# Kernel tuning notes

Hardware: AMD Instinct MI355X
Metric: run time of the kernel (lower is better)

Reference implementation:

```python
import jax, jax.numpy as jnp
import numpy as np

CHANNELS = 1024
N_HEADS = 16
N_EMBD = 512
H_DIM = CHANNELS // N_HEADS


def setup_inputs() -> dict:
    key = jax.random.key(0)
    ks = jax.random.split(key, 10)
    b, hw = 16, 4096
    s = 0.02
    return {
        "x": jax.random.normal(ks[0], (b, hw, CHANNELS), dtype=jnp.float32),
        "p": jax.random.normal(ks[1], (b, 77, N_EMBD), dtype=jnp.float32),
        "Wq": jax.random.normal(ks[2], (CHANNELS, CHANNELS), dtype=jnp.float32) * s,
        "bq": jnp.zeros((CHANNELS,), dtype=jnp.float32),
        "Wk": jax.random.normal(ks[3], (N_EMBD, CHANNELS), dtype=jnp.float32) * s,
        "bk": jnp.zeros((CHANNELS,), dtype=jnp.float32),
        "Wv": jax.random.normal(ks[4], (N_EMBD, CHANNELS), dtype=jnp.float32) * s,
        "bv": jnp.zeros((CHANNELS,), dtype=jnp.float32),
        "Ww": jax.random.normal(ks[5], (CHANNELS, CHANNELS), dtype=jnp.float32) * s,
        "bw": jnp.zeros((CHANNELS,), dtype=jnp.float32),
    }


def reference(x, p, Wq, bq, Wk, bk, Wv, bv, Ww, bw):
    b, hw, c = x.shape
    # Linear projections (torch Linear: y = x @ W^T + b; here weights stored as (in, out))
    q = x @ Wq + bq                      # (b, hw, c)
    k = p @ Wk + bk                      # (b, 77, c)
    v = p @ Wv + bv                      # (b, 77, c)
    q = q.reshape(b, hw, N_HEADS, H_DIM)
    k = k.reshape(b, 77, N_HEADS, H_DIM)
    v = v.reshape(b, 77, N_HEADS, H_DIM)
    scale = 1.0 / jnp.sqrt(jnp.asarray(H_DIM, dtype=x.dtype))
    # scores: (b, heads, hw, 77)
    scores = jnp.einsum("bqhd,bkhd->bhqk", q, k) * scale
    attn = jax.nn.softmax(scores, axis=-1)
    out = jnp.einsum("bhqk,bkhd->bqhd", attn, v).reshape(b, hw, c)
    return out @ Ww + bw
```

## Files before the change

kernel.cpp:

```cpp
#include <hip/hip_runtime.h>
#include <cstdint>
#include <type_traits>

typedef uint16_t u16;
typedef uint32_t u32;
typedef __attribute__((ext_vector_type(4))) float f32x4;
typedef __attribute__((ext_vector_type(8))) __bf16 vbf8;
typedef __attribute__((ext_vector_type(8))) short vs8;

template <typename T, typename = void>
struct CanMfma : std::false_type {};
template <typename T>
struct CanMfma<T, std::void_t<decltype(__builtin_amdgcn_mfma_f32_16x16x32_bf16(
    std::declval<T>(), std::declval<T>(), std::declval<f32x4>(), 0, 0, 0))>>
    : std::true_type {};
typedef std::conditional_t<CanMfma<vbf8>::value, vbf8, vs8> frag_t;

__device__ __forceinline__ f32x4 mfma_bf16(frag_t a, frag_t b, f32x4 c) {
  return __builtin_amdgcn_mfma_f32_16x16x32_bf16(a, b, c, 0, 0, 0);
}

__device__ __forceinline__ u16 f2bf(float f) {
  u32 u = __builtin_bit_cast(u32, f);
  u32 r = (u + 0x7FFFu + ((u >> 16) & 1u)) >> 16;
  return (u16)r;
}

__device__ __forceinline__ void gload_lds16(const void* g, void* l) {
  __builtin_amdgcn_global_load_lds(
      (const __attribute__((address_space(1))) void*)g,
      (__attribute__((address_space(3))) void*)l, 16, 0, 0);
}

__global__ __launch_bounds__(256) void cast_f32_bf16(
    const float* __restrict__ in, u16* __restrict__ out, int n8) {
  int i = blockIdx.x * 256 + threadIdx.x;
  const int stride = gridDim.x * 256;
  for (; i < n8; i += stride) {
    const float4 a  = ((const float4*)in)[(size_t)i * 2];
    const float4 b2 = ((const float4*)in)[(size_t)i * 2 + 1];
    uint4 o;
    o.x = (u32)f2bf(a.x)  | ((u32)f2bf(a.y)  << 16);
    o.y = (u32)f2bf(a.z)  | ((u32)f2bf(a.w)  << 16);
    o.z = (u32)f2bf(b2.x) | ((u32)f2bf(b2.y) << 16);
    o.w = (u32)f2bf(b2.z) | ((u32)f2bf(b2.w) << 16);
    ((uint4*)out)[(size_t)i] = o;
  }
}

__global__ __launch_bounds__(256) void transpose_cast(
    const float* __restrict__ in, u16* __restrict__ out, int K, int N) {
  __shared__ float tile[32][33];
  const int k0 = blockIdx.x * 32, n0 = blockIdx.y * 32;
  const int tr = threadIdx.x >> 5, tc = threadIdx.x & 31;
#pragma unroll
  for (int i = 0; i < 4; ++i)
    tile[tr + i * 8][tc] = in[(size_t)(k0 + tr + i * 8) * N + (n0 + tc)];
  __syncthreads();
#pragma unroll
  for (int i = 0; i < 4; ++i)
    out[(size_t)(n0 + tr + i * 8) * K + (k0 + tc)] = f2bf(tile[tc][tr + i * 8]);
}

template <bool OUT_BF16>
__global__ __launch_bounds__(256) void gemm_bt(
    const u16* __restrict__ A, const u16* __restrict__ Bt,
    const float* __restrict__ bias, void* __restrict__ Cout,
    int M, int N, int K, int Mtiles, int Ntiles) {
  __shared__ char Al[2][128 * 32 * 2];
  __shared__ char Bl[2][128 * 32 * 2];

  const int nwg = Mtiles * Ntiles;
  int bid = (int)blockIdx.x;
  bid = (bid & 7) * (nwg >> 3) + (bid >> 3);
  const int mt = bid / Ntiles, nt = bid % Ntiles;
  const int m0 = mt * 128, n0 = nt * 128;

  const int tid = (int)threadIdx.x;
  const int lane = tid & 63;
  const int wv = tid >> 6;
  const int wm = wv & 1, wn = wv >> 1;
  const int lr = lane & 15, lg = lane >> 4;
  const int rsub = lane >> 2;
  const int slot = lane & 3;
  const int rb0 = n0 + rsub;

  auto stage = [&](int buf, int t) {
    const int k0 = t << 5;
#pragma unroll
    for (int c = 0; c < 2; ++c) {
      const int ci = c * 4 + wv;
      int rra = m0 + ci * 16 + rsub;
      if (rra >= M) rra = M - 1;
      gload_lds16(A + (size_t)rra * K + k0 + slot * 8, Al[buf] + ci * 1024);
      const int rrb = rb0 + ci * 16;
      gload_lds16(Bt + (size_t)rrb * K + k0 + slot * 8, Bl[buf] + ci * 1024);
    }
  };

  f32x4 zero4 = {0.f, 0.f, 0.f, 0.f};
  f32x4 acc[4][4];
#pragma unroll
  for (int i = 0; i < 4; ++i)
#pragma unroll
    for (int j = 0; j < 4; ++j) acc[i][j] = zero4;

  const int nk = K >> 5;
  int cur = 0;
  stage(0, 0);
  __syncthreads();

  for (int t = 0; t < nk; ++t) {
    if (t + 1 < nk) stage(cur ^ 1, t + 1);
    frag_t af[4], bf[4];
#pragma unroll
    for (int i = 0; i < 4; ++i) {
      af[i] = *(const frag_t*)(Al[cur] + (wm * 64 + i * 16 + lr) * 64 + lg * 16);
      bf[i] = *(const frag_t*)(Bl[cur] + (wn * 64 + i * 16 + lr) * 64 + lg * 16);
    }
#pragma unroll
    for (int i = 0; i < 4; ++i)
#pragma unroll
      for (int j = 0; j < 4; ++j)
        acc[i][j] = mfma_bf16(af[i], bf[j], acc[i][j]);
    __syncthreads();
    cur ^= 1;
  }

#pragma unroll
  for (int j = 0; j < 4; ++j) {
    const int col = n0 + wn * 64 + j * 16 + lr;
    const float bv = bias[col];
#pragma unroll
    for (int i = 0; i < 4; ++i) {
      const int rbase = m0 + wm * 64 + i * 16 + lg * 4;
#pragma unroll
      for (int r = 0; r < 4; ++r) {
        const int row = rbase + r;
        const float val = acc[i][j][r] + bv;
        if constexpr (OUT_BF16) {
          u32 me = f2bf(val);
          u32 other = __shfl_xor(me, 1);
          if ((lane & 1) == 0 && row < M) {
            *(u32*)((u16*)Cout + (size_t)row * N + col) = me | (other << 16);
          }
        } else {
          if (row < M) ((float*)Cout)[(size_t)row * N + col] = val;
        }
      }
    }
  }
}

template <bool OUT_BF16>
__global__ __launch_bounds__(512) void gemm256(
    const u16* __restrict__ A, const u16* __restrict__ Bt,
    const float* __restrict__ bias, void* __restrict__ Cout,
    int M, int N, int K) {
  __shared__ u16 Al[2][256 * 64];
  __shared__ u16 Bl[2][256 * 64];

  const int Ntiles = N >> 8;
  const int nwg = (M >> 8) * Ntiles;
  int bid = (int)blockIdx.x;
  bid = (bid & 7) * (nwg >> 3) + (bid >> 3);
  const int mt = bid / Ntiles, ntl = bid % Ntiles;
  const int m0 = mt << 8, n0 = ntl << 8;

  const int tid = (int)threadIdx.x;
  const int lane = tid & 63;
  const int wid = tid >> 6;
  const int wm = wid >> 2, wn = wid & 3;
  const int lr = lane & 15, lg = lane >> 4;
  const int lrx = lr & 7;

  const int chunk = wid * 2;
  const int srow = lane >> 3;
  const int sslot = (lane & 7) ^ srow;
  const u16* Abase = A + (size_t)(m0 + chunk * 8 + srow) * K + sslot * 8;
  const u16* Bbase = Bt + (size_t)(n0 + chunk * 8 + srow) * K + sslot * 8;
  const int ldsChunkByte = (chunk * 8) * 128;

  auto stA = [&](u16* dst, int h, int t) {
    const u16* g = Abase + (size_t)(h << 7) * K + (t << 6);
    char* l = (char*)dst + (h << 14) + ldsChunkByte;
    gload_lds16(g, l);
    gload_lds16(g + ((size_t)K << 3), l + 1024);
  };
  auto stB = [&](u16* dst, int h, int t) {
    const u16* g = Bbase + (size_t)(h << 7) * K + (t << 6);
    char* l = (char*)dst + (h << 14) + ldsChunkByte;
    gload_lds16(g, l);
    gload_lds16(g + ((size_t)K << 3), l + 1024);
  };

  auto ldsF = [&](const u16* base, int row, int ks) -> frag_t {
    return *(const frag_t*)(base + (size_t)row * 64 + ((((ks) << 2) + lg) ^ lrx) * 8);
  };

  f32x4 zero4 = {0.f, 0.f, 0.f, 0.f};
  f32x4 acc[8][4];
#pragma unroll
  for (int i = 0; i < 8; ++i)
#pragma unroll
    for (int j = 0; j < 4; ++j) acc[i][j] = zero4;

  const int nt = K >> 6;
  const int ar0 = wm * 128 + lr;
  const int br0 = wn * 64 + lr;

  stB(&Bl[0][0], 0, 0); stB(&Bl[0][0], 1, 0);
  stA(&Al[0][0], 0, 0); stA(&Al[0][0], 1, 0);
  stB(&Bl[1][0], 0, 1); stB(&Bl[1][0], 1, 1);
  stA(&Al[1][0], 0, 1); stA(&Al[1][0], 1, 1);
  asm volatile("s_waitcnt vmcnt(8)" ::: "memory");
  __builtin_amdgcn_s_barrier();

  for (int t = 0; t < nt; ++t) {
    const int cur = t & 1;
    const u16* al = &Al[cur][0];
    const u16* bl = &Bl[cur][0];
    if (t >= 1 && t + 1 < nt) {
      u16* alN = &Al[cur ^ 1][0];
      u16* blN = &Bl[cur ^ 1][0];
      stB(blN, 0, t + 1); stB(blN, 1, t + 1);
      stA(alN, 0, t + 1); stA(alN, 1, t + 1);
    }
#pragma unroll
    for (int ks = 0; ks < 2; ++ks) {
      frag_t a[8], b[4];
#pragma unroll
      for (int i = 0; i < 8; ++i) a[i] = ldsF(al, ar0 + i * 16, ks);
#pragma unroll
      for (int j = 0; j < 4; ++j) b[j] = ldsF(bl, br0 + j * 16, ks);
#pragma unroll
      for (int i = 0; i < 8; ++i)
#pragma unroll
        for (int j = 0; j < 4; ++j)
          acc[i][j] = mfma_bf16(a[i], b[j], acc[i][j]);
    }
    if (t + 1 < nt) {
      asm volatile("s_waitcnt vmcnt(0)" ::: "memory");
      __builtin_amdgcn_s_barrier();
    }
  }

  float bvv[4];
#pragma unroll
  for (int bj = 0; bj < 4; ++bj) bvv[bj] = bias[n0 + wn * 64 + bj * 16 + lr];
#pragma unroll
  for (int ai = 0; ai < 8; ++ai) {
    const int rbase = m0 + wm * 128 + ai * 16 + lg * 4;
#pragma unroll
    for (int rr = 0; rr < 4; ++rr) {
      const int row = rbase + rr;
#pragma unroll
      for (int bj = 0; bj < 4; ++bj) {
        const int cb = n0 + wn * 64 + bj * 16;
        const float val = acc[ai][bj][rr] + bvv[bj];
        if constexpr (OUT_BF16) {
          u32 me = f2bf(val);
          u32 d0 = me | (__shfl_xor(me, 1) << 16);
          u32 d1 = __shfl_xor(d0, 2);
          if ((lane & 3) == 0) {
            uint2 o; o.x = d0; o.y = d1;
            *(uint2*)((u16*)Cout + (size_t)row * N + cb + (lr & 12)) = o;
          }
        } else {
          float v0 = val;
          float v1 = __shfl_xor(v0, 1);
          float v2 = __shfl_xor(v0, 2);
          float v3 = __shfl_xor(v1, 2);
          if ((lane & 3) == 0) {
            float4 o; o.x = v0; o.y = v1; o.z = v2; o.w = v3;
            *(float4*)((float*)Cout + (size_t)row * N + cb + (lr & 12)) = o;
          }
        }
      }
    }
  }
}

__global__ __launch_bounds__(256) void attn_kernel(
    const u16* __restrict__ Q, const u16* __restrict__ K,
    const u16* __restrict__ V, u16* __restrict__ O) {
  __shared__ u16 Kl[96][72];
  __shared__ u16 Vt[64][104];

  const int bid = blockIdx.x;
  const int qt = bid & 63;
  const int h = (bid >> 6) & 15;
  const int b = bid >> 10;
  const int tid = threadIdx.x;

#pragma unroll
  for (int it = 0; it < 3; ++it) {
    const int idx = tid + it * 256;
    const int key = idx >> 3, s = idx & 7;
    uint4 val{0u, 0u, 0u, 0u};
    if (key < 77)
      val = *(const uint4*)(K + ((size_t)(b * 77 + key)) * 1024 + h * 64 + s * 8);
    *(uint4*)(&Kl[key][s * 8]) = val;
  }
#pragma unroll
  for (int it = 0; it < 3; ++it) {
    const int idx = tid + it * 256;
    if (idx < 616) {
      const int key = idx >> 3, s = idx & 7;
      const uint4 v4 =
          *(const uint4*)(V + ((size_t)(b * 77 + key)) * 1024 + h * 64 + s * 8);
      const u16* e = (const u16*)&v4;
#pragma unroll
      for (int j = 0; j < 8; ++j) Vt[s * 8 + j][key] = e[j];
    }
  }
#pragma unroll
  for (int it = 0; it < 5; ++it) {
    const int idx = tid + it * 256;
    if (idx < 1216) {
      const int d = idx / 19, kk = 77 + idx % 19;
      Vt[d][kk] = 0;
    }
  }
  __syncthreads();

  const int lane = tid & 63;
  const int wv = tid >> 6;
  const int lr = lane & 15;
  const int lg = lane >> 4;

  const size_t qrow = (size_t)(b * 4096 + qt * 64 + wv * 16 + lr) * 1024 + h * 64;
  frag_t qf[2];
#pragma unroll
  for (int ks = 0; ks < 2; ++ks)
    qf[ks] = *(const frag_t*)(Q + qrow + ks * 32 + lg * 8);

  f32x4 zero4 = {0.f, 0.f, 0.f, 0.f};
  f32x4 sa[5] = {zero4, zero4, zero4, zero4, zero4};
#pragma unroll
  for (int ks = 0; ks < 2; ++ks) {
#pragma unroll
    for (int kt = 0; kt < 5; ++kt) {
      frag_t kf = *(const frag_t*)(&Kl[kt * 16 + lr][ks * 32 + lg * 8]);
      sa[kt] = mfma_bf16(kf, qf[ks], sa[kt]);
    }
  }

  float p[5][4];
  float mx = -3.0e38f;
#pragma unroll
  for (int kt = 0; kt < 5; ++kt)
#pragma unroll
    for (int r = 0; r < 4; ++r) {
      const int key = kt * 16 + lg * 4 + r;
      float s = sa[kt][r] * 0.125f;
      if (key >= 77) s = -3.0e38f;
      p[kt][r] = s;
      mx = fmaxf(mx, s);
    }
  mx = fmaxf(mx, __shfl_xor(mx, 16));
  mx = fmaxf(mx, __shfl_xor(mx, 32));
  float sum = 0.f;
#pragma unroll
  for (int kt = 0; kt < 5; ++kt)
#pragma unroll
    for (int r = 0; r < 4; ++r) {
      const float e = __expf(p[kt][r] - mx);
      p[kt][r] = e;
      sum += e;
    }
  sum += __shfl_xor(sum, 16);
  sum += __shfl_xor(sum, 32);
  const float rden = 1.0f / sum;
#pragma unroll
  for (int kt = 0; kt < 5; ++kt)
#pragma unroll
    for (int r = 0; r < 4; ++r) p[kt][r] *= rden;

  union FP { frag_t v; u16 e[8]; };
  frag_t pa[3];
#pragma unroll
  for (int kb = 0; kb < 3; ++kb) {
    FP f;
#pragma unroll
    for (int j = 0; j < 8; ++j) {
      const int kt = 2 * kb + (j >> 2);
      f.e[j] = (kt < 5) ? f2bf(p[kt][j & 3]) : (u16)0;
    }
    pa[kb] = f.v;
  }

  f32x4 oa[4] = {zero4, zero4, zero4, zero4};
#pragma unroll
  for (int nt = 0; nt < 4; ++nt) {
    const int d = nt * 16 + lr;
#pragma unroll
    for (int kb = 0; kb < 3; ++kb) {
      const int key0 = kb * 32 + lg * 4;
      FP vb;
      *(uint2*)(&vb.e[0]) = *(const uint2*)(&Vt[d][key0]);
      *(uint2*)(&vb.e[4]) = *(const uint2*)(&Vt[d][key0 + 16]);
      oa[nt] = mfma_bf16(pa[kb], vb.v, oa[nt]);
    }
  }

#pragma unroll
  for (int nt = 0; nt < 4; ++nt)
#pragma unroll
    for (int r = 0; r < 4; ++r) {
      const int qr = wv * 16 + lg * 4 + r;
      u32 me = f2bf(oa[nt][r]);
      u32 other = __shfl_xor(me, 1);
      if ((lane & 1) == 0) {
        *(u32*)(O + ((size_t)(b * 4096 + qt * 64 + qr)) * 1024 + h * 64 +
                nt * 16 + lr) = me | (other << 16);
      }
    }
}

extern "C" void kernel_launch(void* const* d_in, const int* in_sizes, int n_in,
                              void* d_out, int out_size, void* d_ws, size_t ws_size,
                              hipStream_t stream) {
  const float* x  = (const float*)d_in[0];
  const float* p  = (const float*)d_in[1];
  const float* Wq = (const float*)d_in[2];
  const float* bq = (const float*)d_in[3];
  const float* Wk = (const float*)d_in[4];
  const float* bk = (const float*)d_in[5];
  const float* Wv = (const float*)d_in[6];
  const float* bv = (const float*)d_in[7];
  const float* Ww = (const float*)d_in[8];
  const float* bw = (const float*)d_in[9];

  char* ws = (char*)d_ws;
  if (ws_size < 281034752ULL) return;

  u16* x_bf = (u16*)(ws + 0);
  u16* q_bf = (u16*)(ws + 134217728);
  u16* wq_t = (u16*)(ws + 268435456);
  u16* ww_t = (u16*)(ws + 270532608);
  u16* wk_t = (u16*)(ws + 272629760);
  u16* wv_t = (u16*)(ws + 273678336);
  u16* p_bf = (u16*)(ws + 274726912);
  u16* k_bf = (u16*)(ws + 275988480);
  u16* v_bf = (u16*)(ws + 278511616);

  cast_f32_bf16<<<4096, 256, 0, stream>>>(x, x_bf, 8388608);
  cast_f32_bf16<<<308, 256, 0, stream>>>(p, p_bf, 78848);
  transpose_cast<<<dim3(32, 32), 256, 0, stream>>>(Wq, wq_t, 1024, 1024);
  transpose_cast<<<dim3(32, 32), 256, 0, stream>>>(Ww, ww_t, 1024, 1024);
  transpose_cast<<<dim3(16, 32), 256, 0, stream>>>(Wk, wk_t, 512, 1024);
  transpose_cast<<<dim3(16, 32), 256, 0, stream>>>(Wv, wv_t, 512, 1024);

  gemm_bt<true><<<80, 256, 0, stream>>>(p_bf, wk_t, bk, k_bf, 1232, 1024, 512, 10, 8);
  gemm_bt<true><<<80, 256, 0, stream>>>(p_bf, wv_t, bv, v_bf, 1232, 1024, 512, 10, 8);
  gemm256<true><<<1024, 512, 0, stream>>>(x_bf, wq_t, bq, q_bf, 65536, 1024, 1024);
  attn_kernel<<<16384, 256, 0, stream>>>(q_bf, k_bf, v_bf, x_bf);
  gemm256<false><<<1024, 512, 0, stream>>>(x_bf, ww_t, bw, d_out, 65536, 1024, 1024);
}
```

Measured before the change: 622.9 us.

## Fuse fp32-to-bf16 cast of x into the Q projection GEMM A-load

Removes the standalone cast kernel over x. The Q GEMM now loads fp32 A tiles into registers, converts them to bf16, and writes them swizzled into LDS. This saves a full write and re-read of a 128MB bf16 copy, but the GEMM now reads fp32 A from global memory, which doubles A traffic, and pays for register staging and conversion. The prologue also changes: only stage 0 is prefetched, the next tile is issued every iteration, and the bf16 path waits with vmcnt(0) instead of keeping two stages in flight.

```diff
diff --git a/kernel.cpp b/kernel.cpp
--- a/kernel.cpp
+++ b/kernel.cpp
@@ -31,6 +31,8 @@
       (const __attribute__((address_space(1))) void*)g,
       (__attribute__((address_space(3))) void*)l, 16, 0, 0);
 }
+
+#define VMW0() asm volatile("s_waitcnt vmcnt(0)" ::: "memory")
 
 __global__ __launch_bounds__(256) void cast_f32_bf16(
     const float* __restrict__ in, u16* __restrict__ out, int n8) {
@@ -152,13 +154,16 @@
   }
 }
 
-template <bool OUT_BF16>
+template <bool OUT_BF16, bool A_F32>
 __global__ __launch_bounds__(512) void gemm256(
-    const u16* __restrict__ A, const u16* __restrict__ Bt,
+    const void* __restrict__ Ain, const u16* __restrict__ Bt,
     const float* __restrict__ bias, void* __restrict__ Cout,
     int M, int N, int K) {
   __shared__ u16 Al[2][256 * 64];
   __shared__ u16 Bl[2][256 * 64];
+
+  const u16* A16 = (const u16*)Ain;
+  const float* A32 = (const float*)Ain;
 
   const int Ntiles = N >> 8;
   const int nwg = (M >> 8) * Ntiles;
@@ -177,7 +182,8 @@
   const int chunk = wid * 2;
   const int srow = lane >> 3;
   const int sslot = (lane & 7) ^ srow;
-  const u16* Abase = A + (size_t)(m0 + chunk * 8 + srow) * K + sslot * 8;
+  const u16* Abase = A_F32 ? nullptr
+                           : A16 + (size_t)(m0 + chunk * 8 + srow) * K + sslot * 8;
   const u16* Bbase = Bt + (size_t)(n0 + chunk * 8 + srow) * K + sslot * 8;
   const int ldsChunkByte = (chunk * 8) * 128;
 
@@ -194,6 +200,34 @@
     gload_lds16(g + ((size_t)K << 3), l + 1024);
   };
 
+  float4 areg[8];
+  auto issueA32 = [&](int t) {
+#pragma unroll
+    for (int h = 0; h < 2; ++h)
+#pragma unroll
+      for (int ps = 0; ps < 4; ++ps) {
+        const int row = m0 + h * 128 + ps * 32 + (tid >> 4);
+        areg[h * 4 + ps] =
+            *(const float4*)(A32 + (size_t)row * K + t * 64 + (tid & 15) * 4);
+      }
+  };
+  auto writeA32 = [&](u16* dst) {
+    const int slot16 = (tid & 15) >> 1;
+    const int half8 = tid & 1;
+#pragma unroll
+    for (int h = 0; h < 2; ++h)
+#pragma unroll
+      for (int ps = 0; ps < 4; ++ps) {
+        const int rowL = h * 128 + ps * 32 + (tid >> 4);
+        const float4 v = areg[h * 4 + ps];
+        uint2 o;
+        o.x = (u32)f2bf(v.x) | ((u32)f2bf(v.y) << 16);
+        o.y = (u32)f2bf(v.z) | ((u32)f2bf(v.w) << 16);
+        const int phys = slot16 ^ (rowL & 7);
+        *(uint2*)((char*)dst + rowL * 128 + phys * 16 + half8 * 8) = o;
+      }
+  };
+
   auto ldsF = [&](const u16* base, int row, int ks) -> frag_t {
     return *(const frag_t*)(base + (size_t)row * 64 + ((((ks) << 2) + lg) ^ lrx) * 8);
   };
@@ -210,21 +244,32 @@
   const int br0 = wn * 64 + lr;
 
   stB(&Bl[0][0], 0, 0); stB(&Bl[0][0], 1, 0);
-  stA(&Al[0][0], 0, 0); stA(&Al[0][0], 1, 0);
-  stB(&Bl[1][0], 0, 1); stB(&Bl[1][0], 1, 1);
-  stA(&Al[1][0], 0, 1); stA(&Al[1][0], 1, 1);
-  asm volatile("s_waitcnt vmcnt(8)" ::: "memory");
-  __builtin_amdgcn_s_barrier();
+  if constexpr (A_F32) {
+    issueA32(0);
+    VMW0();
+    writeA32(&Al[0][0]);
+    __syncthreads();
+  } else {
+    stA(&Al[0][0], 0, 0); stA(&Al[0][0], 1, 0);
+    VMW0();
+    __builtin_amdgcn_s_barrier();
+  }
 
   for (int t = 0; t < nt; ++t) {
     const int cur = t & 1;
     const u16* al = &Al[cur][0];
     const u16* bl = &Bl[cur][0];
-    if (t >= 1 && t + 1 < nt) {
+    const bool more = (t + 1 < nt);
+    if (more) {
       u16* alN = &Al[cur ^ 1][0];
       u16* blN = &Bl[cur ^ 1][0];
       stB(blN, 0, t + 1); stB(blN, 1, t + 1);
-      stA(alN, 0, t + 1); stA(alN, 1, t + 1);
+      if constexpr (A_F32) {
+        issueA32(t + 1);
+        (void)alN;
+      } else {
+        stA(alN, 0, t + 1); stA(alN, 1, t + 1);
+      }
     }
 #pragma unroll
     for (int ks = 0; ks < 2; ++ks) {
@@ -239,9 +284,14 @@
         for (int j = 0; j < 4; ++j)
           acc[i][j] = mfma_bf16(a[i], b[j], acc[i][j]);
     }
-    if (t + 1 < nt) {
-      asm volatile("s_waitcnt vmcnt(0)" ::: "memory");
-      __builtin_amdgcn_s_barrier();
+    if (more) {
+      VMW0();
+      if constexpr (A_F32) {
+        writeA32(&Al[cur ^ 1][0]);
+        __syncthreads();
+      } else {
+        __builtin_amdgcn_s_barrier();
+      }
     }
   }
 
@@ -435,7 +485,7 @@
   char* ws = (char*)d_ws;
   if (ws_size < 281034752ULL) return;
 
-  u16* x_bf = (u16*)(ws + 0);
+  u16* ao_bf = (u16*)(ws + 0);
   u16* q_bf = (u16*)(ws + 134217728);
   u16* wq_t = (u16*)(ws + 268435456);
   u16* ww_t = (u16*)(ws + 270532608);
@@ -445,7 +495,6 @@
   u16* k_bf = (u16*)(ws + 275988480);
   u16* v_bf = (u16*)(ws + 278511616);
 
-  cast_f32_bf16<<<4096, 256, 0, stream>>>(x, x_bf, 8388608);
   cast_f32_bf16<<<308, 256, 0, stream>>>(p, p_bf, 78848);
   transpose_cast<<<dim3(32, 32), 256, 0, stream>>>(Wq, wq_t, 1024, 1024);
   transpose_cast<<<dim3(32, 32), 256, 0, stream>>>(Ww, ww_t, 1024, 1024);
@@ -454,7 +503,7 @@
 
   gemm_bt<true><<<80, 256, 0, stream>>>(p_bf, wk_t, bk, k_bf, 1232, 1024, 512, 10, 8);
   gemm_bt<true><<<80, 256, 0, stream>>>(p_bf, wv_t, bv, v_bf, 1232, 1024, 512, 10, 8);
-  gemm256<true><<<1024, 512, 0, stream>>>(x_bf, wq_t, bq, q_bf, 65536, 1024, 1024);
-  attn_kernel<<<16384, 256, 0, stream>>>(q_bf, k_bf, v_bf, x_bf);
-  gemm256<false><<<1024, 512, 0, stream>>>(x_bf, ww_t, bw, d_out, 65536, 1024, 1024);
-}
+  gemm256<true, true><<<1024, 512, 0, stream>>>(x, wq_t, bq, q_bf, 65536, 1024, 1024);
+  attn_kernel<<<16384, 256, 0, stream>>>(q_bf, k_bf, v_bf, ao_bf);
+  gemm256<false, false><<<1024, 512, 0, stream>>>(ao_bf, ww_t, bw, d_out, 65536, 1024, 1024);
+}
```

After: 645.2 us. 3.6% more time.

## Shrink gemm256 tile to 256x128 with K-step 32 for higher occupancy

Applied to the files above, without the earlier changes.

The large GEMM kernel moves from 256x256 tiles with a 64-wide K step to 256x128 tiles with a 32-wide K step. Waves are rearranged as a 4x2 grid, each owning a 64x64 sub-tile, and the LDS staging and XOR swizzle are redone to match. LDS use and accumulator registers per block drop, and launch bounds now ask for 4 blocks per CU, which aims to raise occupancy and latency hiding. The costs are lower arithmetic intensity, more B-tile reloads, and twice as many barriers per K, with grid size doubled to match.

```diff
diff --git a/kernel.cpp b/kernel.cpp
--- a/kernel.cpp
+++ b/kernel.cpp
@@ -153,92 +153,75 @@
 }
 
 template <bool OUT_BF16>
-__global__ __launch_bounds__(512) void gemm256(
+__global__ __launch_bounds__(512, 4) void gemm256(
     const u16* __restrict__ A, const u16* __restrict__ Bt,
     const float* __restrict__ bias, void* __restrict__ Cout,
     int M, int N, int K) {
-  __shared__ u16 Al[2][256 * 64];
-  __shared__ u16 Bl[2][256 * 64];
-
-  const int Ntiles = N >> 8;
+  __shared__ u16 Al[2][256 * 32];
+  __shared__ u16 Bl[2][128 * 32];
+
+  const int Ntiles = N >> 7;
   const int nwg = (M >> 8) * Ntiles;
   int bid = (int)blockIdx.x;
   bid = (bid & 7) * (nwg >> 3) + (bid >> 3);
   const int mt = bid / Ntiles, ntl = bid % Ntiles;
-  const int m0 = mt << 8, n0 = ntl << 8;
+  const int m0 = mt << 8, n0 = ntl << 7;
 
   const int tid = (int)threadIdx.x;
   const int lane = tid & 63;
   const int wid = tid >> 6;
-  const int wm = wid >> 2, wn = wid & 3;
+  const int wm = wid >> 1, wn = wid & 1;
   const int lr = lane & 15, lg = lane >> 4;
-  const int lrx = lr & 7;
-
-  const int chunk = wid * 2;
-  const int srow = lane >> 3;
-  const int sslot = (lane & 7) ^ srow;
-  const u16* Abase = A + (size_t)(m0 + chunk * 8 + srow) * K + sslot * 8;
-  const u16* Bbase = Bt + (size_t)(n0 + chunk * 8 + srow) * K + sslot * 8;
-  const int ldsChunkByte = (chunk * 8) * 128;
-
-  auto stA = [&](u16* dst, int h, int t) {
-    const u16* g = Abase + (size_t)(h << 7) * K + (t << 6);
-    char* l = (char*)dst + (h << 14) + ldsChunkByte;
-    gload_lds16(g, l);
-    gload_lds16(g + ((size_t)K << 3), l + 1024);
+
+  const int srow = lane >> 2;
+  const int sslot = (lane & 3) ^ ((lane >> 3) & 3);
+  const u16* Abase = A + (size_t)(m0 + wid * 32 + srow) * K + sslot * 8;
+  const u16* Bbase = Bt + (size_t)(n0 + wid * 16 + srow) * K + sslot * 8;
+
+  auto stage = [&](u16* da, u16* db, int t) {
+    const int k0 = t << 5;
+    gload_lds16(Abase + k0, (char*)da + wid * 2048);
+    gload_lds16(Abase + ((size_t)K << 4) + k0, (char*)da + wid * 2048 + 1024);
+    gload_lds16(Bbase + k0, (char*)db + wid * 1024);
   };
-  auto stB = [&](u16* dst, int h, int t) {
-    const u16* g = Bbase + (size_t)(h << 7) * K + (t << 6);
-    char* l = (char*)dst + (h << 14) + ldsChunkByte;
-    gload_lds16(g, l);
-    gload_lds16(g + ((size_t)K << 3), l + 1024);
+
+  auto ldsF = [&](const u16* base, int row) -> frag_t {
+    const int phys = lg ^ ((row >> 1) & 3);
+    return *(const frag_t*)(base + (size_t)row * 32 + phys * 8);
   };
 
-  auto ldsF = [&](const u16* base, int row, int ks) -> frag_t {
-    return *(const frag_t*)(base + (size_t)row * 64 + ((((ks) << 2) + lg) ^ lrx) * 8);
-  };
-
   f32x4 zero4 = {0.f, 0.f, 0.f, 0.f};
-  f32x4 acc[8][4];
-#pragma unroll
-  for (int i = 0; i < 8; ++i)
+  f32x4 acc[4][4];
+#pragma unroll
+  for (int i = 0; i < 4; ++i)
 #pragma unroll
     for (int j = 0; j < 4; ++j) acc[i][j] = zero4;
 
-  const int nt = K >> 6;
-  const int ar0 = wm * 128 + lr;
+  const int nt = K >> 5;
+  const int ar0 = wm * 64 + lr;
   const int br0 = wn * 64 + lr;
 
-  stB(&Bl[0][0], 0, 0); stB(&Bl[0][0], 1, 0);
-  stA(&Al[0][0], 0, 0); stA(&Al[0][0], 1, 0);
-  stB(&Bl[1][0], 0, 1); stB(&Bl[1][0], 1, 1);
-  stA(&Al[1][0], 0, 1); stA(&Al[1][0], 1, 1);
-  asm volatile("s_waitcnt vmcnt(8)" ::: "memory");
+  stage(&Al[0][0], &Bl[0][0], 0);
+  stage(&Al[1][0], &Bl[1][0], 1);
+  asm volatile("s_waitcnt vmcnt(3)" ::: "memory");
   __builtin_amdgcn_s_barrier();
 
   for (int t = 0; t < nt; ++t) {
     const int cur = t & 1;
     const u16* al = &Al[cur][0];
     const u16* bl = &Bl[cur][0];
-    if (t >= 1 && t + 1 < nt) {
-      u16* alN = &Al[cur ^ 1][0];
-      u16* blN = &Bl[cur ^ 1][0];
-      stB(blN, 0, t + 1); stB(blN, 1, t + 1);
-      stA(alN, 0, t + 1); stA(alN, 1, t + 1);
-    }
-#pragma unroll
-    for (int ks = 0; ks < 2; ++ks) {
-      frag_t a[8], b[4];
-#pragma unroll
-      for (int i = 0; i < 8; ++i) a[i] = ldsF(al, ar0 + i * 16, ks);
-#pragma unroll
-      for (int j = 0; j < 4; ++j) b[j] = ldsF(bl, br0 + j * 16, ks);
-#pragma unroll
-      for (int i = 0; i < 8; ++i)
-#pragma unroll
-        for (int j = 0; j < 4; ++j)
-          acc[i][j] = mfma_bf16(a[i], b[j], acc[i][j]);
-    }
+    if (t >= 1 && t + 1 < nt)
+      stage(&Al[cur ^ 1][0], &Bl[cur ^ 1][0], t + 1);
+    frag_t a[4], b[4];
+#pragma unroll
+    for (int i = 0; i < 4; ++i) a[i] = ldsF(al, ar0 + i * 16);
+#pragma unroll
+    for (int j = 0; j < 4; ++j) b[j] = ldsF(bl, br0 + j * 16);
+#pragma unroll
+    for (int i = 0; i < 4; ++i)
+#pragma unroll
+      for (int j = 0; j < 4; ++j)
+        acc[i][j] = mfma_bf16(a[i], b[j], acc[i][j]);
     if (t + 1 < nt) {
       asm volatile("s_waitcnt vmcnt(0)" ::: "memory");
       __builtin_amdgcn_s_barrier();
@@ -249,8 +232,8 @@
 #pragma unroll
   for (int bj = 0; bj < 4; ++bj) bvv[bj] = bias[n0 + wn * 64 + bj * 16 + lr];
 #pragma unroll
-  for (int ai = 0; ai < 8; ++ai) {
-    const int rbase = m0 + wm * 128 + ai * 16 + lg * 4;
+  for (int ai = 0; ai < 4; ++ai) {
+    const int rbase = m0 + wm * 64 + ai * 16 + lg * 4;
 #pragma unroll
     for (int rr = 0; rr < 4; ++rr) {
       const int row = rbase + rr;
@@ -454,7 +437,7 @@
 
   gemm_bt<true><<<80, 256, 0, stream>>>(p_bf, wk_t, bk, k_bf, 1232, 1024, 512, 10, 8);
   gemm_bt<true><<<80, 256, 0, stream>>>(p_bf, wv_t, bv, v_bf, 1232, 1024, 512, 10, 8);
-  gemm256<true><<<1024, 512, 0, stream>>>(x_bf, wq_t, bq, q_bf, 65536, 1024, 1024);
+  gemm256<true><<<2048, 512, 0, stream>>>(x_bf, wq_t, bq, q_bf, 65536, 1024, 1024);
   attn_kernel<<<16384, 256, 0, stream>>>(q_bf, k_bf, v_bf, x_bf);
-  gemm256<false><<<1024, 512, 0, stream>>>(x_bf, ww_t, bw, d_out, 65536, 1024, 1024);
-}
+  gemm256<false><<<2048, 512, 0, stream>>>(x_bf, ww_t, bw, d_out, 65536, 1024, 1024);
+}
```

Measured after the change: 633.9 us. No clear change (+1.8%).
